# Performance work log

Measured on AMD Instinct MI355X. Metric: run time of the kernel, lower is better.

Reference implementation:

```python
import jax, jax.numpy as jnp
import numpy as np

V, P, C, M, P_ORIG, T = 81920, 131072, 512, 1024, 163840, 262144


def setup_inputs() -> dict:
    key = jax.random.key(0)
    ks = jax.random.split(key, 6)
    adapter_feat = jax.random.normal(ks[0], (V, C), dtype=jnp.float32)
    ce = jax.random.normal(ks[1], (M, C), dtype=jnp.float32)
    # caption embeddings arrive pre-normalized in the original pipeline
    caption_embed = ce / jnp.clip(jnp.linalg.norm(ce, axis=-1, keepdims=True), 1e-12)
    logit_scale = jnp.full((1,), np.log(1.0 / 0.07), dtype=jnp.float32)  # learnable param init
    v2p_map = jax.random.randint(ks[2], (P,), 0, V, dtype=jnp.int32)
    origin_idx = jax.random.randint(ks[3], (P,), 0, P_ORIG, dtype=jnp.int32)
    caption_to_point_mapping = jax.random.randint(ks[4], (T,), 0, P_ORIG, dtype=jnp.int32)
    caption_seg_idx = jnp.sort(jax.random.randint(ks[5], (T,), 0, M, dtype=jnp.int32))
    return {
        "adapter_feat": adapter_feat,
        "caption_embed": caption_embed,
        "logit_scale": logit_scale,
        "v2p_map": v2p_map,
        "origin_idx": origin_idx,
        "caption_to_point_mapping": caption_to_point_mapping,
        "caption_seg_idx": caption_seg_idx,
        "n_origin_points": P_ORIG,
    }


def reference(adapter_feat, caption_embed, logit_scale, v2p_map, origin_idx,
              caption_to_point_mapping, caption_seg_idx, n_origin_points):
    n_pts = v2p_map.shape[0]
    n_captions = caption_embed.shape[0]

    # gather voxel features to points, L2-normalize (feat_norm=True)
    feats = adapter_feat[v2p_map]                                       # [P, C]
    feats = feats / jnp.clip(jnp.linalg.norm(feats, axis=-1, keepdims=True), 1e-12)

    # per-point log-softmax caption scores
    logits = (feats @ caption_embed.T) * jnp.exp(logit_scale[0])        # [P, M]
    scores = jax.nn.log_softmax(logits, axis=-1)                        # [P, M]

    # origin-point -> current-point mapping; -1 where origin point was dropped
    ptom = jnp.full((n_origin_points,), -1, dtype=jnp.int32)
    ptom = ptom.at[origin_idx].set(jnp.arange(n_pts, dtype=jnp.int32))

    gidx = ptom[caption_to_point_mapping]                               # [T]
    invalid = (gidx < 0).astype(scores.dtype)                           # [T]
    # torch negative advanced indexing wraps; replicate faithfully
    safe = jnp.where(gidx < 0, gidx + n_pts, gidx)
    gathered = scores[safe]                                             # [T, M]

    # scatter-sum scores and counts per caption segment
    pooled = jax.ops.segment_sum(gathered, caption_seg_idx, num_segments=n_captions)
    cnt = jax.ops.segment_sum(jnp.ones_like(invalid), caption_seg_idx, num_segments=n_captions)
    ninv = jax.ops.segment_sum(invalid, caption_seg_idx, num_segments=n_captions)
    real_n_points = cnt - ninv                                          # [N]

    denom = jnp.where(real_n_points > 0,
                      1.0 / jnp.where(real_n_points > 0, real_n_points, 1.0), 0.0)
    pooled = pooled * denom[:, None]                                    # [N, M]
    if_has_pts = real_n_points > 0
    return pooled, real_n_points, if_has_pts
```

## Files before the change

kernel.cpp:

```cpp
#include <hip/hip_runtime.h>

#define P_PTS 131072
#define CDIM  512
#define MCAP  1024
#define TLEN  262144
#define PORIG 163840

typedef unsigned short u16;
typedef unsigned char  u8;
typedef __attribute__((ext_vector_type(8))) short short8;
typedef __attribute__((ext_vector_type(4))) float f32x4;
typedef __attribute__((ext_vector_type(8))) int int8v;
typedef __attribute__((ext_vector_type(4))) int int4v;

__device__ __forceinline__ u16 f2bf(float f) {
    unsigned u = __float_as_uint(f);
    unsigned r = (u + 0x7FFFu + ((u >> 16) & 1u)) >> 16;
    return (u16)r;
}
__device__ __forceinline__ float d_e4m3(unsigned x) {
    float f = __uint_as_float((x & 0x7Fu) << 20) * 0x1p120f;
    return __uint_as_float(__float_as_uint(f) | ((x & 0x80u) << 24));
}


__global__ __launch_bounds__(256) void gather_prep(
    const float* __restrict__ adapter, const int* __restrict__ v2p,
    const float* __restrict__ cap, const int* __restrict__ oidx,
    u8* __restrict__ feats8, u16* __restrict__ capb, u8* __restrict__ Bswz,
    int* __restrict__ ptom, float* __restrict__ lse_sum) {
    __shared__ __align__(16) u8 sm[4 * 544];
    int b = blockIdx.x, tid = threadIdx.x;
    if (b < 32768) {
        int w = tid >> 6, lane = tid & 63;
        int p = b * 4 + w;
        int vrow = v2p[p];
        const float4* src = (const float4*)(adapter + (size_t)vrow * CDIM);
        float4 x0 = src[lane * 2];
        float4 x1 = src[lane * 2 + 1];
        float ss = x0.x*x0.x + x0.y*x0.y + x0.z*x0.z + x0.w*x0.w
                 + x1.x*x1.x + x1.y*x1.y + x1.z*x1.z + x1.w*x1.w;
        #pragma unroll
        for (int off = 32; off >= 1; off >>= 1) ss += __shfl_xor(ss, off, 64);
        float inv = 1.0f / fmaxf(sqrtf(ss), 1e-12f);
        int lo = __builtin_amdgcn_cvt_pk_fp8_f32(x0.x*inv, x0.y*inv, 0, false);
        lo = __builtin_amdgcn_cvt_pk_fp8_f32(x0.z*inv, x0.w*inv, lo, true);
        int hi = __builtin_amdgcn_cvt_pk_fp8_f32(x1.x*inv, x1.y*inv, 0, false);
        hi = __builtin_amdgcn_cvt_pk_fp8_f32(x1.z*inv, x1.w*inv, hi, true);
        uint2 wv; wv.x = (unsigned)lo; wv.y = (unsigned)hi;
        *(uint2*)(sm + w * 544 + lane * 8) = wv;
        __syncthreads();
        int chunk = tid >> 4, inner = tid & 15;
        int kk = chunk >> 2, q = chunk & 3, rr = inner >> 2;
        uint2 v = *(const uint2*)(sm + rr * 544 + kk * 128 + q * 32 + (inner & 3) * 8);
        *(uint2*)(feats8 + (size_t)(b >> 2) * 8192 + kk * 2048 + q * 512
                         + (b & 3) * 128 + inner * 8) = v;
    } else if (b < 33280) {
        int t = (b - 32768) * 256 + tid;
        int i = t * 4;
        float4 v = *(const float4*)(cap + i);
        u16* o = capb + i;
        o[0] = f2bf(v.x); o[1] = f2bf(v.y); o[2] = f2bf(v.z); o[3] = f2bf(v.w);
        atomicMax(&ptom[oidx[t]], t);
    } else if (b < 33792) {
        int j = (b - 33280) * 256 + tid;
        lse_sum[j] = 0.0f;
    } else {
        int g2 = (b - 33792) * 256 + tid;
        int c    = g2 & 1;
        int lane = (g2 >> 1) & 63;
        int j    = (g2 >> 7) & 3;
        int kk   = (g2 >> 9) & 3;
        int wn   = (g2 >> 11) & 1;
        int c0   = g2 >> 12;
        int col  = c0 * 128 + wn * 64 + j * 16 + (lane & 15);
        int kb   = kk * 128 + (lane >> 4) * 32 + c * 16;
        const float* s = cap + (size_t)col * CDIM + kb;
        unsigned w4[4];
        #pragma unroll
        for (int u = 0; u < 4; ++u) {
            int p = __builtin_amdgcn_cvt_pk_fp8_f32(s[u*4+0], s[u*4+1], 0, false);
            p = __builtin_amdgcn_cvt_pk_fp8_f32(s[u*4+2], s[u*4+3], p, true);
            w4[u] = (unsigned)p;
        }
        *(uint4*)(Bswz + (size_t)g2 * 16) = *(uint4*)w4;
    }
}

__global__ __launch_bounds__(256) void lse_gemm(
    const u8* __restrict__ feats8, const u8* __restrict__ Bswz,
    const float* __restrict__ lsc, float* __restrict__ lse_sum,
    const int* __restrict__ ctpm, const int* __restrict__ ptom,
    unsigned* __restrict__ rows) {
    if (blockIdx.x >= 8192) {
        int t = (blockIdx.x - 8192) * 256 + threadIdx.x;
        int g = ptom[ctpm[t]];
        rows[t] = (g < 0) ? ((unsigned)(g + P_PTS) | 0x80000000u) : (unsigned)g;
        return;
    }
    const int tid  = threadIdx.x;
    const int wave = tid >> 6;
    const int lane = tid & 63;
    const unsigned id = blockIdx.x;
    const int c0   = (int)((id >> 3) & 7u);
    const int row0 = (int)((id & 7u) + 8u * (id >> 6)) * 128;
    const int wm = (wave >> 1) * 64;
    const int wn1 = (wave & 1);
    const float sf = __expf(lsc[0]);

    f32x4 acc[4][4] = {};

    const int m = lane & 15;
    const int q = lane >> 4;
    const u8* gA = feats8 + (size_t)(row0 + wm) * CDIM + lane * 32;
    const u8* bw = Bswz + (size_t)(c0 * 2 + wn1) * 16 * 2048 + lane * 32;

    #pragma unroll
    for (int k0 = 0; k0 < CDIM; k0 += 128) {
        const int kk = k0 >> 7;
        int8v bv[4];
        #pragma unroll
        for (int j = 0; j < 4; ++j) {
            int4v lo = *(const int4v*)(bw + (kk * 4 + j) * 2048);
            int4v hi = *(const int4v*)(bw + (kk * 4 + j) * 2048 + 16);
            bv[j][0]=lo[0]; bv[j][1]=lo[1]; bv[j][2]=lo[2]; bv[j][3]=lo[3];
            bv[j][4]=hi[0]; bv[j][5]=hi[1]; bv[j][6]=hi[2]; bv[j][7]=hi[3];
        }
        int8v af[4];
        #pragma unroll
        for (int i = 0; i < 4; ++i) {
            const u8* a = gA + i * 8192 + kk * 2048;
            int4v lo = *(const int4v*)(a);
            int4v hi = *(const int4v*)(a + 16);
            af[i][0]=lo[0]; af[i][1]=lo[1]; af[i][2]=lo[2]; af[i][3]=lo[3];
            af[i][4]=hi[0]; af[i][5]=hi[1]; af[i][6]=hi[2]; af[i][7]=hi[3];
        }
        #pragma unroll
        for (int i = 0; i < 4; ++i)
            #pragma unroll
            for (int j = 0; j < 4; ++j)
                acc[i][j] = __builtin_amdgcn_mfma_scale_f32_16x16x128_f8f6f4(
                    af[i], bv[j], acc[i][j], 0, 0, 0, 127, 0, 127);
    }

    #pragma unroll
    for (int i = 0; i < 4; ++i) {
        float s4[4] = {0.f, 0.f, 0.f, 0.f};
        #pragma unroll
        for (int j = 0; j < 4; ++j)
            #pragma unroll
            for (int r = 0; r < 4; ++r)
                s4[r] += __expf(acc[i][j][r] * sf - sf);
        #pragma unroll
        for (int off = 8; off >= 1; off >>= 1)
            #pragma unroll
            for (int r = 0; r < 4; ++r)
                s4[r] += __shfl_xor(s4[r], off, 64);
        if (m == 0) {
            int rbase = row0 + wm + i * 16 + q * 4;
            #pragma unroll
            for (int r = 0; r < 4; ++r)
                atomicAdd(&lse_sum[rbase + r], s4[r]);
        }
    }
}

__device__ __forceinline__ int lower_bound(const int* __restrict__ a, int n, int key) {
    int lo = 0, hi = n;
    while (lo < hi) { int mid = (lo + hi) >> 1; if (a[mid] < key) lo = mid + 1; else hi = mid; }
    return lo;
}

__global__ __launch_bounds__(1024) void seg_reduce(
    const u8* __restrict__ feats8, const float* __restrict__ lse_sum,
    const unsigned* __restrict__ rows, const int* __restrict__ seg,
    const float* __restrict__ lsc,
    u16* __restrict__ Fb, float* __restrict__ Lout, float* __restrict__ realn) {
    int s = blockIdx.x;
    int tid = threadIdx.x, wave = tid >> 6, lane = tid & 63;
    int start = lower_bound(seg, TLEN, s);
    int end   = lower_bound(seg, TLEN, s + 1);
    const int loff = (lane >> 4) * 2048 + ((lane >> 2) & 3) * 512 + (lane & 3) * 8;
    const int chb  = (lane >> 4) * 128  + ((lane >> 2) & 3) * 32  + (lane & 3) * 8;
    float a[8] = {0,0,0,0,0,0,0,0};
    float Lacc = 0.f; int inv = 0;
    int r = start + wave;
    for (; r + 16 < end; r += 32) {
        unsigned p0 = rows[r], p1 = rows[r + 16];
        int r0 = (int)(p0 & 0x7FFFFFFFu), r1 = (int)(p1 & 0x7FFFFFFFu);
        uint2 v0 = *(const uint2*)(feats8 + (size_t)(r0 >> 4) * 8192 + (r0 & 15) * 32 + loff);
        uint2 v1 = *(const uint2*)(feats8 + (size_t)(r1 >> 4) * 8192 + (r1 & 15) * 32 + loff);
        if (lane == 0) {
            inv += (int)(p0 >> 31) + (int)(p1 >> 31);
            Lacc += __logf(lse_sum[r0]) + __logf(lse_sum[r1]);
        }
        a[0] += d_e4m3(v0.x);       a[1] += d_e4m3(v0.x >> 8);
        a[2] += d_e4m3(v0.x >> 16); a[3] += d_e4m3(v0.x >> 24);
        a[4] += d_e4m3(v0.y);       a[5] += d_e4m3(v0.y >> 8);
        a[6] += d_e4m3(v0.y >> 16); a[7] += d_e4m3(v0.y >> 24);
        a[0] += d_e4m3(v1.x);       a[1] += d_e4m3(v1.x >> 8);
        a[2] += d_e4m3(v1.x >> 16); a[3] += d_e4m3(v1.x >> 24);
        a[4] += d_e4m3(v1.y);       a[5] += d_e4m3(v1.y >> 8);
        a[6] += d_e4m3(v1.y >> 16); a[7] += d_e4m3(v1.y >> 24);
    }
    if (r < end) {
        unsigned p0 = rows[r];
        int r0 = (int)(p0 & 0x7FFFFFFFu);
        uint2 v0 = *(const uint2*)(feats8 + (size_t)(r0 >> 4) * 8192 + (r0 & 15) * 32 + loff);
        if (lane == 0) { inv += (int)(p0 >> 31); Lacc += __logf(lse_sum[r0]); }
        a[0] += d_e4m3(v0.x);       a[1] += d_e4m3(v0.x >> 8);
        a[2] += d_e4m3(v0.x >> 16); a[3] += d_e4m3(v0.x >> 24);
        a[4] += d_e4m3(v0.y);       a[5] += d_e4m3(v0.y >> 8);
        a[6] += d_e4m3(v0.y >> 16); a[7] += d_e4m3(v0.y >> 24);
    }
    __shared__ float pF[16][512];
    __shared__ float pL[16];
    __shared__ int   pI[16];
    #pragma unroll
    for (int u = 0; u < 8; ++u) pF[wave][chb + u] = a[u];
    if (lane == 0) { pL[wave] = Lacc; pI[wave] = inv; }
    __syncthreads();
    if (tid < 512) {
        float f = 0.f;
        #pragma unroll
        for (int w = 0; w < 16; ++w) f += pF[w][tid];
        Fb[(size_t)s * CDIM + tid] = f2bf(f);
    }
    if (tid == 0) {
        float cnt = (float)(end - start);
        float Ls = 0.f; int ninv = 0;
        #pragma unroll
        for (int w = 0; w < 16; ++w) { Ls += pL[w]; ninv += pI[w]; }
        realn[s] = cnt - (float)ninv;
        Lout[s] = Ls + __expf(lsc[0]) * cnt;
    }
}

__global__ __launch_bounds__(256) void pooled_gemm(
    const u16* __restrict__ Fb, const u16* __restrict__ capb,
    const float* __restrict__ Lout, const float* __restrict__ realn,
    const float* __restrict__ lsc, float* __restrict__ out) {
    const int tid  = threadIdx.x;
    const int wave = tid >> 6;
    const int lane = tid & 63;
    const int col0 = blockIdx.x * 64;
    const int row0 = blockIdx.y * 64;
    const int wm = (wave >> 1) * 32;
    const int wn = (wave & 1) * 32;
    const float sf = __expf(lsc[0]);
    f32x4 acc[2][2] = {};
    const int mrow = lane & 15;
    const int quad = lane >> 4;
    const u16* gA = Fb   + (size_t)(row0 + wm + mrow) * CDIM + quad * 8;
    const u16* gB = capb + (size_t)(col0 + wn + mrow) * CDIM + quad * 8;
    #pragma unroll
    for (int k0 = 0; k0 < CDIM; k0 += 32) {
        short8 af[2], bfr[2];
        #pragma unroll
        for (int i = 0; i < 2; ++i)
            af[i]  = *(const short8*)(gA + (size_t)(i * 16) * CDIM + k0);
        #pragma unroll
        for (int j = 0; j < 2; ++j)
            bfr[j] = *(const short8*)(gB + (size_t)(j * 16) * CDIM + k0);
        #pragma unroll
        for (int i = 0; i < 2; ++i)
            #pragma unroll
            for (int j = 0; j < 2; ++j)
                acc[i][j] = __builtin_amdgcn_mfma_f32_16x16x32_bf16(
                    af[i], bfr[j], acc[i][j], 0, 0, 0);
    }
    #pragma unroll
    for (int i = 0; i < 2; ++i) {
        #pragma unroll
        for (int r = 0; r < 4; ++r) {
            int s = row0 + wm + i * 16 + quad * 4 + r;
            float rn = realn[s];
            float dn = rn > 0.f ? 1.0f / rn : 0.0f;
            float L = Lout[s];
            #pragma unroll
            for (int j = 0; j < 2; ++j) {
                int mc = col0 + wn + j * 16 + mrow;
                out[(size_t)s * MCAP + mc] = (sf * acc[i][j][r] - L) * dn;
            }
        }
    }
    if (col0 == 0 && tid < 64) {
        int s = row0 + tid;
        float rv = realn[s];
        out[MCAP * MCAP + s] = rv;
        out[MCAP * MCAP + MCAP + s] = (rv > 0.f) ? 1.0f : 0.0f;
    }
}

extern "C" void kernel_launch(void* const* d_in, const int* in_sizes, int n_in,
                              void* d_out, int out_size, void* d_ws, size_t ws_size,
                              hipStream_t stream) {
    const float* adapter = (const float*)d_in[0];
    const float* cap     = (const float*)d_in[1];
    const float* lsc     = (const float*)d_in[2];
    const int*   v2p     = (const int*)d_in[3];
    const int*   oidx    = (const int*)d_in[4];
    const int*   ctpm    = (const int*)d_in[5];
    const int*   seg     = (const int*)d_in[6];
    float* out = (float*)d_out;

    char* ws = (char*)d_ws;
    u8*       feats8  = (u8*)(ws);
    u16*      capb    = (u16*)(ws + 67108864);
    u8*       Bswz    = (u8*)(ws + 68157440);
    float*    lse_sum = (float*)(ws + 68681728);
    int*      ptom    = (int*)(ws + 69206016);
    unsigned* rows    = (unsigned*)(ws + 69861376);
    u16*      Fb      = (u16*)(ws + 70909952);
    float*    Lout    = (float*)(ws + 71958528);
    float*    realn   = (float*)(ws + 71962624);

    hipMemsetAsync(ptom, 0xFF, (size_t)PORIG * 4, stream);

    gather_prep<<<33920, 256, 0, stream>>>(adapter, v2p, cap, oidx,
                                           feats8, capb, Bswz, ptom, lse_sum);
    lse_gemm<<<8192 + TLEN / 256, 256, 0, stream>>>(feats8, Bswz, lsc, lse_sum,
                                                    ctpm, ptom, rows);
    seg_reduce<<<MCAP, 1024, 0, stream>>>(feats8, lse_sum, rows, seg, lsc, Fb, Lout, realn);
    pooled_gemm<<<dim3(MCAP / 64, MCAP / 64), 256, 0, stream>>>(Fb, capb, Lout, realn, lsc, out);
}
```

Before: 430.7 us.

## Stage A row tile in LDS and loop all caption columns per block

Each lse_gemm block now owns a 128-row slab and loops over all 8 caption column tiles, staging its fp8 A tile once in LDS via global_load_lds instead of re-reading A from global for every column tile. The per-row exp sums are accumulated in registers and written directly, replacing the atomicAdds across column blocks. This cuts A re-reads and atomic traffic but leaves only 1024 GEMM blocks, each with 64KB of LDS, which limits occupancy and latency hiding. The B operand is still read from global.

```diff
diff --git a/kernel.cpp b/kernel.cpp
--- a/kernel.cpp
+++ b/kernel.cpp
@@ -21,6 +21,11 @@
 __device__ __forceinline__ float d_e4m3(unsigned x) {
     float f = __uint_as_float((x & 0x7Fu) << 20) * 0x1p120f;
     return __uint_as_float(__float_as_uint(f) | ((x & 0x80u) << 24));
+}
+__device__ __forceinline__ void ld16(const void* g, void* l) {
+    __builtin_amdgcn_global_load_lds(
+        (const __attribute__((address_space(1))) void*)g,
+        (__attribute__((address_space(3))) void*)l, 16, 0, 0);
 }
 
 
@@ -87,80 +92,107 @@
     }
 }
 
-__global__ __launch_bounds__(256) void lse_gemm(
+__global__ __launch_bounds__(256, 2) void lse_gemm(
     const u8* __restrict__ feats8, const u8* __restrict__ Bswz,
     const float* __restrict__ lsc, float* __restrict__ lse_sum,
     const int* __restrict__ ctpm, const int* __restrict__ ptom,
     unsigned* __restrict__ rows) {
-    if (blockIdx.x >= 8192) {
-        int t = (blockIdx.x - 8192) * 256 + threadIdx.x;
+    if (blockIdx.x >= 1024) {
+        int t = (blockIdx.x - 1024) * 256 + threadIdx.x;
         int g = ptom[ctpm[t]];
         rows[t] = (g < 0) ? ((unsigned)(g + P_PTS) | 0x80000000u) : (unsigned)g;
         return;
     }
+    __shared__ __align__(16) u8 As[65536];
     const int tid  = threadIdx.x;
     const int wave = tid >> 6;
     const int lane = tid & 63;
-    const unsigned id = blockIdx.x;
-    const int c0   = (int)((id >> 3) & 7u);
-    const int row0 = (int)((id & 7u) + 8u * (id >> 6)) * 128;
-    const int wm = (wave >> 1) * 64;
-    const int wn1 = (wave & 1);
+    const int bid  = blockIdx.x;
+    const int row0 = bid * 128;
+    const int wm   = (wave >> 1) * 64;
+    const int wn1  = (wave & 1);
     const float sf = __expf(lsc[0]);
 
-    f32x4 acc[4][4] = {};
+    {
+        const u8* src = feats8 + (size_t)(bid * 8 + wave * 2) * 8192 + lane * 16;
+        u8* dst = As + wave * 2 * 8192;
+        #pragma unroll
+        for (int cr = 0; cr < 2; ++cr)
+            #pragma unroll
+            for (int kk = 0; kk < 4; ++kk) {
+                ld16(src + cr * 8192 + kk * 2048,        dst + cr * 8192 + kk * 2048);
+                ld16(src + cr * 8192 + kk * 2048 + 1024, dst + cr * 8192 + kk * 2048 + 1024);
+            }
+    }
+    asm volatile("s_waitcnt vmcnt(0)" ::: "memory");
+    __builtin_amdgcn_sched_barrier(0);
+    __builtin_amdgcn_s_barrier();
+    __builtin_amdgcn_sched_barrier(0);
 
     const int m = lane & 15;
     const int q = lane >> 4;
-    const u8* gA = feats8 + (size_t)(row0 + wm) * CDIM + lane * 32;
-    const u8* bw = Bswz + (size_t)(c0 * 2 + wn1) * 16 * 2048 + lane * 32;
-
+    const u8* rA = As + (size_t)(wave >> 1) * 32768 + lane * 32;
+
+    float ssum[4][4];
     #pragma unroll
-    for (int k0 = 0; k0 < CDIM; k0 += 128) {
-        const int kk = k0 >> 7;
-        int8v bv[4];
-        #pragma unroll
-        for (int j = 0; j < 4; ++j) {
-            int4v lo = *(const int4v*)(bw + (kk * 4 + j) * 2048);
-            int4v hi = *(const int4v*)(bw + (kk * 4 + j) * 2048 + 16);
-            bv[j][0]=lo[0]; bv[j][1]=lo[1]; bv[j][2]=lo[2]; bv[j][3]=lo[3];
-            bv[j][4]=hi[0]; bv[j][5]=hi[1]; bv[j][6]=hi[2]; bv[j][7]=hi[3];
-        }
-        int8v af[4];
+    for (int i = 0; i < 4; ++i)
+        #pragma unroll
+        for (int r = 0; r < 4; ++r) ssum[i][r] = 0.f;
+
+    #pragma unroll 1
+    for (int c0 = 0; c0 < 8; ++c0) {
+        const u8* bw = Bswz + (size_t)(c0 * 2 + wn1) * 32768 + lane * 32;
+        f32x4 acc[4][4] = {};
+        #pragma unroll
+        for (int kk = 0; kk < 4; ++kk) {
+            int8v bv[4];
+            #pragma unroll
+            for (int j = 0; j < 4; ++j) {
+                int4v lo = *(const int4v*)(bw + (kk * 4 + j) * 2048);
+                int4v hi = *(const int4v*)(bw + (kk * 4 + j) * 2048 + 16);
+                bv[j][0]=lo[0]; bv[j][1]=lo[1]; bv[j][2]=lo[2]; bv[j][3]=lo[3];
+                bv[j][4]=hi[0]; bv[j][5]=hi[1]; bv[j][6]=hi[2]; bv[j][7]=hi[3];
+            }
+            int8v af[4];
+            #pragma unroll
+            for (int i = 0; i < 4; ++i) {
+                const u8* a = rA + i * 8192 + kk * 2048;
+                int4v lo = *(const int4v*)(a);
+                int4v hi = *(const int4v*)(a + 16);
+                af[i][0]=lo[0]; af[i][1]=lo[1]; af[i][2]=lo[2]; af[i][3]=lo[3];
+                af[i][4]=hi[0]; af[i][5]=hi[1]; af[i][6]=hi[2]; af[i][7]=hi[3];
+            }
+            #pragma unroll
+            for (int i = 0; i < 4; ++i)
+                #pragma unroll
+                for (int j = 0; j < 4; ++j)
+                    acc[i][j] = __builtin_amdgcn_mfma_scale_f32_16x16x128_f8f6f4(
+                        af[i], bv[j], acc[i][j], 0, 0, 0, 127, 0, 127);
+        }
         #pragma unroll
         for (int i = 0; i < 4; ++i) {
-            const u8* a = gA + i * 8192 + kk * 2048;
-            int4v lo = *(const int4v*)(a);
-            int4v hi = *(const int4v*)(a + 16);
-            af[i][0]=lo[0]; af[i][1]=lo[1]; af[i][2]=lo[2]; af[i][3]=lo[3];
-            af[i][4]=hi[0]; af[i][5]=hi[1]; af[i][6]=hi[2]; af[i][7]=hi[3];
-        }
-        #pragma unroll
-        for (int i = 0; i < 4; ++i)
+            float s4[4] = {0.f, 0.f, 0.f, 0.f};
             #pragma unroll
             for (int j = 0; j < 4; ++j)
-                acc[i][j] = __builtin_amdgcn_mfma_scale_f32_16x16x128_f8f6f4(
-                    af[i], bv[j], acc[i][j], 0, 0, 0, 127, 0, 127);
-    }
-
-    #pragma unroll
-    for (int i = 0; i < 4; ++i) {
-        float s4[4] = {0.f, 0.f, 0.f, 0.f};
-        #pragma unroll
-        for (int j = 0; j < 4; ++j)
+                #pragma unroll
+                for (int r = 0; r < 4; ++r)
+                    s4[r] += __expf(acc[i][j][r] * sf - sf);
+            #pragma unroll
+            for (int off = 8; off >= 1; off >>= 1)
+                #pragma unroll
+                for (int r = 0; r < 4; ++r)
+                    s4[r] += __shfl_xor(s4[r], off, 64);
+            #pragma unroll
+            for (int r = 0; r < 4; ++r) ssum[i][r] += s4[r];
+        }
+    }
+    if (m == 0) {
+        #pragma unroll
+        for (int i = 0; i < 4; ++i) {
+            int rbase = row0 + wm + i * 16 + q * 4;
             #pragma unroll
             for (int r = 0; r < 4; ++r)
-                s4[r] += __expf(acc[i][j][r] * sf - sf);
-        #pragma unroll
-        for (int off = 8; off >= 1; off >>= 1)
-            #pragma unroll
-            for (int r = 0; r < 4; ++r)
-                s4[r] += __shfl_xor(s4[r], off, 64);
-        if (m == 0) {
-            int rbase = row0 + wm + i * 16 + q * 4;
-            #pragma unroll
-            for (int r = 0; r < 4; ++r)
-                atomicAdd(&lse_sum[rbase + r], s4[r]);
+                lse_sum[rbase + r] = ssum[i][r];
         }
     }
 }
@@ -319,7 +351,7 @@
 
     gather_prep<<<33920, 256, 0, stream>>>(adapter, v2p, cap, oidx,
                                            feats8, capb, Bswz, ptom, lse_sum);
-    lse_gemm<<<8192 + TLEN / 256, 256, 0, stream>>>(feats8, Bswz, lsc, lse_sum,
+    lse_gemm<<<1024 + TLEN / 256, 256, 0, stream>>>(feats8, Bswz, lsc, lse_sum,
                                                     ctpm, ptom, rows);
     seg_reduce<<<MCAP, 1024, 0, stream>>>(feats8, lse_sum, rows, seg, lsc, Fb, Lout, realn);
     pooled_gemm<<<dim3(MCAP / 64, MCAP / 64), 256, 0, stream>>>(Fb, capb, Lout, realn, lsc, out);
```

Result: no change. 424.4 us (-1.5%).

## Double-buffer A tiles in LDS via async global_load_lds in lse_gemm

Applied to the files above, without the earlier changes.

The lse_gemm kernel now stages A-operand (fp8 feature) tiles into a double-buffered LDS array with direct global-to-LDS loads. The next K-slice is prefetched while MFMAs run on the current one, and each wave reads its fragments from LDS. Previously A was loaded straight from global memory into registers inside each k-step, and the two waves sharing rows loaded them twice. It also adds a launch-bounds occupancy hint, at the cost of 32KB of LDS per block and a barrier every k-step.

```diff
diff --git a/kernel.cpp b/kernel.cpp
--- a/kernel.cpp
+++ b/kernel.cpp
@@ -13,6 +13,8 @@
 typedef __attribute__((ext_vector_type(8))) int int8v;
 typedef __attribute__((ext_vector_type(4))) int int4v;
 
+union V32 { int8v v8; int4v v4[2]; };
+
 __device__ __forceinline__ u16 f2bf(float f) {
     unsigned u = __float_as_uint(f);
     unsigned r = (u + 0x7FFFu + ((u >> 16) & 1u)) >> 16;
@@ -21,6 +23,11 @@
 __device__ __forceinline__ float d_e4m3(unsigned x) {
     float f = __uint_as_float((x & 0x7Fu) << 20) * 0x1p120f;
     return __uint_as_float(__float_as_uint(f) | ((x & 0x80u) << 24));
+}
+__device__ __forceinline__ void ld16(const void* g, void* l) {
+    __builtin_amdgcn_global_load_lds(
+        (const __attribute__((address_space(1))) void*)g,
+        (__attribute__((address_space(3))) void*)l, 16, 0, 0);
 }
 
 
@@ -87,7 +94,7 @@
     }
 }
 
-__global__ __launch_bounds__(256) void lse_gemm(
+__global__ __launch_bounds__(256, 4) void lse_gemm(
     const u8* __restrict__ feats8, const u8* __restrict__ Bswz,
     const float* __restrict__ lsc, float* __restrict__ lse_sum,
     const int* __restrict__ ctpm, const int* __restrict__ ptom,
@@ -98,51 +105,64 @@
         rows[t] = (g < 0) ? ((unsigned)(g + P_PTS) | 0x80000000u) : (unsigned)g;
         return;
     }
+    __shared__ __align__(16) u8 As[2][16384];
     const int tid  = threadIdx.x;
     const int wave = tid >> 6;
     const int lane = tid & 63;
     const unsigned id = blockIdx.x;
     const int c0   = (int)((id >> 3) & 7u);
-    const int row0 = (int)((id & 7u) + 8u * (id >> 6)) * 128;
-    const int wm = (wave >> 1) * 64;
-    const int wn1 = (wave & 1);
+    const int rt   = (int)((id & 7u) + 8u * (id >> 6));
+    const int row0 = rt * 128;
+    const int wm   = (wave >> 1) * 64;
+    const int wn1  = (wave & 1);
     const float sf = __expf(lsc[0]);
 
+    const u8* gAb = feats8 + ((size_t)rt * 8 + wave * 2) * 8192 + lane * 16;
+    #define STAGE(KK, BUF)                                                    \
+        {   u8* d = As[BUF] + wave * 4096;                                    \
+            _Pragma("unroll")                                                 \
+            for (int u = 0; u < 4; ++u)                                       \
+                ld16(gAb + (size_t)(u >> 1) * 8192 + (KK) * 2048 + (u & 1) * 1024, \
+                     d + u * 1024); }
+
+    const u8* rA0 = As[0] + (size_t)((wave >> 1) * 4) * 2048 + lane * 32;
+    const u8* rA1 = As[1] + (size_t)((wave >> 1) * 4) * 2048 + lane * 32;
+    const u8* bw = Bswz + (size_t)(c0 * 2 + wn1) * 32768 + lane * 32;
+
     f32x4 acc[4][4] = {};
+
+    STAGE(0, 0)
+    __syncthreads();
+
+    #pragma unroll
+    for (int kk = 0; kk < 4; ++kk) {
+        if (kk < 3) {
+            if (kk & 1) { STAGE(kk + 1, 0) } else { STAGE(kk + 1, 1) }
+        }
+        const u8* rA = (kk & 1) ? rA1 : rA0;
+        int8v bv[4];
+        #pragma unroll
+        for (int j = 0; j < 4; ++j) {
+            int4v lo = *(const int4v*)(bw + kk * 8192 + j * 2048);
+            int4v hi = *(const int4v*)(bw + kk * 8192 + j * 2048 + 16);
+            bv[j][0]=lo[0]; bv[j][1]=lo[1]; bv[j][2]=lo[2]; bv[j][3]=lo[3];
+            bv[j][4]=hi[0]; bv[j][5]=hi[1]; bv[j][6]=hi[2]; bv[j][7]=hi[3];
+        }
+        #pragma unroll
+        for (int i = 0; i < 4; ++i) {
+            V32 af;
+            af.v4[0] = *(const int4v*)(rA + i * 2048);
+            af.v4[1] = *(const int4v*)(rA + i * 2048 + 16);
+            #pragma unroll
+            for (int j = 0; j < 4; ++j)
+                acc[i][j] = __builtin_amdgcn_mfma_scale_f32_16x16x128_f8f6f4(
+                    af.v8, bv[j], acc[i][j], 0, 0, 0, 127, 0, 127);
+        }
+        __syncthreads();
+    }
 
     const int m = lane & 15;
     const int q = lane >> 4;
-    const u8* gA = feats8 + (size_t)(row0 + wm) * CDIM + lane * 32;
-    const u8* bw = Bswz + (size_t)(c0 * 2 + wn1) * 16 * 2048 + lane * 32;
-
-    #pragma unroll
-    for (int k0 = 0; k0 < CDIM; k0 += 128) {
-        const int kk = k0 >> 7;
-        int8v bv[4];
-        #pragma unroll
-        for (int j = 0; j < 4; ++j) {
-            int4v lo = *(const int4v*)(bw + (kk * 4 + j) * 2048);
-            int4v hi = *(const int4v*)(bw + (kk * 4 + j) * 2048 + 16);
-            bv[j][0]=lo[0]; bv[j][1]=lo[1]; bv[j][2]=lo[2]; bv[j][3]=lo[3];
-            bv[j][4]=hi[0]; bv[j][5]=hi[1]; bv[j][6]=hi[2]; bv[j][7]=hi[3];
-        }
-        int8v af[4];
-        #pragma unroll
-        for (int i = 0; i < 4; ++i) {
-            const u8* a = gA + i * 8192 + kk * 2048;
-            int4v lo = *(const int4v*)(a);
-            int4v hi = *(const int4v*)(a + 16);
-            af[i][0]=lo[0]; af[i][1]=lo[1]; af[i][2]=lo[2]; af[i][3]=lo[3];
-            af[i][4]=hi[0]; af[i][5]=hi[1]; af[i][6]=hi[2]; af[i][7]=hi[3];
-        }
-        #pragma unroll
-        for (int i = 0; i < 4; ++i)
-            #pragma unroll
-            for (int j = 0; j < 4; ++j)
-                acc[i][j] = __builtin_amdgcn_mfma_scale_f32_16x16x128_f8f6f4(
-                    af[i], bv[j], acc[i][j], 0, 0, 0, 127, 0, 127);
-    }
-
     #pragma unroll
     for (int i = 0; i < 4; ++i) {
         float s4[4] = {0.f, 0.f, 0.f, 0.f};
@@ -163,6 +183,7 @@
                 atomicAdd(&lse_sum[rbase + r], s4[r]);
         }
     }
+    #undef STAGE
 }
 
 __device__ __forceinline__ int lower_bound(const int* __restrict__ a, int n, int key) {
```

Measured after the change: 531.0 us. 23.3% more time.
